# Performance work log

Measured on AMD Instinct MI355X. Metric: run time of the kernel, lower is better.

Reference implementation:

```python
import jax, jax.numpy as jnp
import numpy as np

EPS = 1e-6
BLK = 16  # NVFP4 block size (16 elements share one e4m3 scale)
# e2m1 representable magnitudes and rounding midpoints
GRID = jnp.array([0.0, 0.5, 1.0, 1.5, 2.0, 3.0, 4.0, 6.0], dtype=jnp.float32)
MID = jnp.array([0.25, 0.75, 1.25, 1.75, 2.5, 3.5, 5.0], dtype=jnp.float32)


def _e2m1(x):
    # round magnitude to nearest e2m1 grid point (saturate at 6.0)
    a = jnp.minimum(jnp.abs(x), 6.0)
    idx = jnp.searchsorted(MID, a, side='right')
    return jnp.sign(x) * jnp.take(GRID, idx)


def _fp4_quant_scaled(x, gscale):
    # vllm scaled_fp4_quant: per-16 block amax -> e4m3 block scale (scaled by
    # global scale), quantize to e2m1. Returns q * s8 (= dequant * gscale).
    m, n = x.shape
    xb = x.reshape(m, n // BLK, BLK)
    amax = jnp.max(jnp.abs(xb), axis=-1, keepdims=True)
    s8 = (amax * gscale / 6.0).astype(jnp.float8_e4m3fn).astype(jnp.float32)
    safe = jnp.where(s8 > 0, s8, 1.0)
    q = _e2m1(jnp.where(s8 > 0, xb * gscale / safe, 0.0))
    return (q * s8).reshape(m, n)


def _fp4_mm(y, w, ag, wg):
    # cutlass_scaled_fp4_mm with alpha = 1/(ag*wg): dequantized matmul y @ w.T
    alpha = 1.0 / (ag * wg)
    yq = _fp4_quant_scaled(y, ag)   # [m, h]
    wq = _fp4_quant_scaled(w, wg)   # [h, h]
    return (yq @ wq.T) * alpha


def _rmsnorm(x, w):
    v = jnp.mean(x * x, axis=-1, keepdims=True)
    return x * jax.lax.rsqrt(v + EPS) * w


def setup_inputs() -> dict:
    key = jax.random.key(0)
    k1, k2, k3, k4 = jax.random.split(key, 4)
    T, H = 8192, 4096
    hidden_states = jax.random.normal(k1, (T, H), dtype=jnp.float32)
    norm_w = jnp.ones((4, H), dtype=jnp.float32)          # RMSNorm weights (init ones)
    w = jax.random.uniform(k2, (3, H, H), dtype=jnp.float32)     # torch.rand
    agscale = jax.random.uniform(k3, (3,), dtype=jnp.float32, minval=0.25, maxval=1.0)
    wgscale = jax.random.uniform(k4, (3,), dtype=jnp.float32, minval=0.25, maxval=1.0)
    return {"hidden_states": hidden_states, "norm_w": norm_w, "w": w,
            "agscale": agscale, "wgscale": wgscale}


def reference(hidden_states, norm_w, w, agscale, wgscale):
    # tensor_model_parallel_all_reduce == identity on a single device
    x = jnp.maximum(hidden_states, 0.0)  # relu
    resid = x
    y = _rmsnorm(x, norm_w[0])
    for i in range(3):  # 3 structurally distinct layers (fixed small loop)
        z = _fp4_mm(y, w[i], agscale[i], wgscale[i])
        resid = z + resid                # fused add
        y = _rmsnorm(resid, norm_w[i + 1])
    return y
```

## Files before the change

kernel.cpp:

```cpp
#include <hip/hip_runtime.h>
#include <stdint.h>

#define HD 4096
#define TD 8192

typedef unsigned short u16;
typedef unsigned int u32;
typedef __bf16 bf16x8 __attribute__((ext_vector_type(8)));
typedef float f32x4 __attribute__((ext_vector_type(4)));

#define GL16(gp, lp) __builtin_amdgcn_global_load_lds( \
    (__attribute__((address_space(1))) void*)(void*)(uintptr_t)(gp), \
    (__attribute__((address_space(3))) void*)(lp), 16, 0, 0)


__device__ __forceinline__ float e4m3_rtne(float f) {
  if (f <= 0.0f) return 0.0f;
  unsigned u = __float_as_uint(f);
  int e = (int)((u >> 23) & 0xff) - 127;
  if (e < -6) e = -6;
  float C = __uint_as_float((unsigned)(e + 147) << 23);
  float r = (f + C) - C;
  return fminf(r, 448.0f);
}

__device__ __forceinline__ void quant_store16(const float v[16], float g, u16* dst) {
  float amax = 0.0f;
#pragma unroll
  for (int j = 0; j < 16; ++j) amax = fmaxf(amax, fabsf(v[j]));
  float s = e4m3_rtne(amax * g / 6.0f);
  u32 out[8];
  if (s > 0.0f) {
    const float m1 = 0.25f * s, m2 = 0.75f * s, m3 = 1.25f * s, m4 = 1.75f * s;
    const float m5 = 2.5f * s, m6 = 3.5f * s, m7 = 5.0f * s;
#pragma unroll
    for (int p = 0; p < 8; ++p) {
      u16 b[2];
#pragma unroll
      for (int h = 0; h < 2; ++h) {
        float t = v[2 * p + h] * g;
        float u = fabsf(t);
        float q = (u < m4) ? ((u < m2) ? ((u < m1) ? 0.0f : 0.5f)
                                       : ((u < m3) ? 1.0f : 1.5f))
                           : ((u < m6) ? ((u < m5) ? 2.0f : 3.0f)
                                       : ((u < m7) ? 4.0f : 6.0f));
        float val = copysignf(q * s, t);
        b[h] = (u16)(__float_as_uint(val) >> 16);
      }
      out[p] = (u32)b[0] | ((u32)b[1] << 16);
    }
  } else {
#pragma unroll
    for (int p = 0; p < 8; ++p) out[p] = 0u;
  }
  uint4* d4 = (uint4*)dst;
  d4[0] = make_uint4(out[0], out[1], out[2], out[3]);
  d4[1] = make_uint4(out[4], out[5], out[6], out[7]);
}

__device__ __forceinline__ float block_sum256(float v) {
#pragma unroll
  for (int off = 32; off > 0; off >>= 1) v += __shfl_down(v, off, 64);
  __shared__ float red[4];
  int tid = threadIdx.x;
  if ((tid & 63) == 0) red[tid >> 6] = v;
  __syncthreads();
  return (red[0] + red[1]) + (red[2] + red[3]);
}


__global__ __launch_bounds__(256) void k_relu_norm_quant(
    const float* __restrict__ hs, const float* __restrict__ nw,
    const float* __restrict__ agp, float* __restrict__ resid,
    u16* __restrict__ yq) {
  const int row = blockIdx.x, tid = threadIdx.x;
  const size_t base = (size_t)row * HD + tid * 16;
  float v[16];
#pragma unroll
  for (int j = 0; j < 4; ++j) ((float4*)v)[j] = ((const float4*)(hs + base))[j];
  float ss = 0.0f;
#pragma unroll
  for (int j = 0; j < 16; ++j) {
    v[j] = fmaxf(v[j], 0.0f);
    ss += v[j] * v[j];
  }
#pragma unroll
  for (int j = 0; j < 4; ++j) ((float4*)(resid + base))[j] = ((float4*)v)[j];
  float tot = block_sum256(ss);
  float rs = 1.0f / sqrtf(tot * (1.0f / HD) + 1e-6f);
  const float* nwp = nw + tid * 16;
  float y[16];
#pragma unroll
  for (int j = 0; j < 16; ++j) y[j] = v[j] * rs * nwp[j];
  quant_store16(y, agp[0], yq + base);
}

__global__ __launch_bounds__(256) void k_norm_quant(
    const float* __restrict__ resid, const float* __restrict__ nw,
    const float* __restrict__ agp, int li, u16* __restrict__ yq) {
  const int row = blockIdx.x, tid = threadIdx.x;
  const size_t base = (size_t)row * HD + tid * 16;
  float v[16];
#pragma unroll
  for (int j = 0; j < 4; ++j) ((float4*)v)[j] = ((const float4*)(resid + base))[j];
  float ss = 0.0f;
#pragma unroll
  for (int j = 0; j < 16; ++j) ss += v[j] * v[j];
  float tot = block_sum256(ss);
  float rs = 1.0f / sqrtf(tot * (1.0f / HD) + 1e-6f);
  const float* nwp = nw + (size_t)li * HD + tid * 16;
  float y[16];
#pragma unroll
  for (int j = 0; j < 16; ++j) y[j] = v[j] * rs * nwp[j];
  quant_store16(y, agp[li], yq + base);
}

__global__ __launch_bounds__(256) void k_final_norm(
    float* __restrict__ io, const float* __restrict__ nw) {
  const int row = blockIdx.x, tid = threadIdx.x;
  const size_t base = (size_t)row * HD + tid * 16;
  float v[16];
#pragma unroll
  for (int j = 0; j < 4; ++j) ((float4*)v)[j] = ((const float4*)(io + base))[j];
  float ss = 0.0f;
#pragma unroll
  for (int j = 0; j < 16; ++j) ss += v[j] * v[j];
  float tot = block_sum256(ss);
  float rs = 1.0f / sqrtf(tot * (1.0f / HD) + 1e-6f);
  const float* nwp = nw + (size_t)3 * HD + tid * 16;
#pragma unroll
  for (int j = 0; j < 16; ++j) v[j] = v[j] * rs * nwp[j];
#pragma unroll
  for (int j = 0; j < 4; ++j) ((float4*)(io + base))[j] = ((float4*)v)[j];
}

__global__ __launch_bounds__(256) void k_quant_w(
    const float* __restrict__ w, const float* __restrict__ wgp, int li,
    u16* __restrict__ wq) {
  const int row = blockIdx.x, tid = threadIdx.x;
  const size_t base = (size_t)li * HD * HD + (size_t)row * HD + tid * 16;
  float v[16];
#pragma unroll
  for (int j = 0; j < 4; ++j) ((float4*)v)[j] = ((const float4*)(w + base))[j];
  quant_store16(v, wgp[li], wq + (size_t)row * HD + tid * 16);
}


__global__ __launch_bounds__(256, 5) void k_gemm(
    const u16* __restrict__ A, const u16* __restrict__ B,
    float* __restrict__ resid, const float* __restrict__ agp,
    const float* __restrict__ wgp, int layer) {
  __shared__ __align__(16) u16 ldsA[128 * 32];
  __shared__ __align__(16) u16 ldsB[128 * 32];
  const int tid = threadIdx.x;
  const int wave = tid >> 6, lane = tid & 63;
  const int m0 = blockIdx.y * 128, n0 = blockIdx.x * 128;

  const int c0 = wave * 64 + lane;
  const int c1 = c0 + 256;
  const int rA0 = c0 >> 2, col0 = ((c0 & 3) ^ ((c0 >> 3) & 3)) * 8;
  const int rA1 = c1 >> 2, col1 = ((c1 & 3) ^ ((c1 >> 3) & 3)) * 8;

  const u16* gA0 = A + (size_t)(m0 + rA0) * HD + col0;
  const u16* gA1 = A + (size_t)(m0 + rA1) * HD + col1;
  const u16* gB0 = B + (size_t)(n0 + rA0) * HD + col0;
  const u16* gB1 = B + (size_t)(n0 + rA1) * HD + col1;
  u16* lA0 = ldsA + c0 * 8;
  u16* lA1 = ldsA + c1 * 8;
  u16* lB0 = ldsB + c0 * 8;
  u16* lB1 = ldsB + c1 * 8;

  const int wm = (wave >> 1) * 64, wn = (wave & 1) * 64;
  const int r = lane & 15, q = lane >> 4;
  const int sw = (q ^ ((r >> 1) & 3)) * 8;

  f32x4 acc[4][4];
#pragma unroll
  for (int i = 0; i < 4; ++i)
#pragma unroll
    for (int j = 0; j < 4; ++j) acc[i][j] = (f32x4){0.f, 0.f, 0.f, 0.f};

  for (int k0 = 0; k0 < HD; k0 += 32) {
    __syncthreads();
    GL16(gA0, lA0);
    GL16(gA1, lA1);
    GL16(gB0, lB0);
    GL16(gB1, lB1);
    gA0 += 32; gA1 += 32; gB0 += 32; gB1 += 32;
    __syncthreads();
    bf16x8 a[4], b[4];
#pragma unroll
    for (int i = 0; i < 4; ++i)
      a[i] = *(const bf16x8*)&ldsA[(wm + i * 16 + r) * 32 + sw];
#pragma unroll
    for (int j = 0; j < 4; ++j)
      b[j] = *(const bf16x8*)&ldsB[(wn + j * 16 + r) * 32 + sw];
#pragma unroll
    for (int i = 0; i < 4; ++i)
#pragma unroll
      for (int j = 0; j < 4; ++j)
        acc[i][j] = __builtin_amdgcn_mfma_f32_16x16x32_bf16(a[i], b[j], acc[i][j], 0, 0, 0);
  }

  const float alpha = 1.0f / (agp[layer] * wgp[layer]);
#pragma unroll
  for (int i = 0; i < 4; ++i) {
    const int gm0 = m0 + wm + i * 16 + q * 4;
#pragma unroll
    for (int j = 0; j < 4; ++j) {
      const int gn = n0 + wn + j * 16 + r;
#pragma unroll
      for (int t = 0; t < 4; ++t) {
        float* p = resid + (size_t)(gm0 + t) * HD + gn;
        *p = fmaf(acc[i][j][t], alpha, *p);
      }
    }
  }
}


extern "C" void kernel_launch(void* const* d_in, const int* in_sizes, int n_in,
                              void* d_out, int out_size, void* d_ws, size_t ws_size,
                              hipStream_t stream) {
  const float* hs = (const float*)d_in[0];
  const float* nw = (const float*)d_in[1];
  const float* w = (const float*)d_in[2];
  const float* ag = (const float*)d_in[3];
  const float* wg = (const float*)d_in[4];
  float* out = (float*)d_out;

  u16* wq = (u16*)d_ws;
  u16* yq = (u16*)d_ws + (size_t)HD * HD;

  k_relu_norm_quant<<<TD, 256, 0, stream>>>(hs, nw, ag, out, yq);
  for (int l = 0; l < 3; ++l) {
    k_quant_w<<<HD, 256, 0, stream>>>(w, wg, l, wq);
    k_gemm<<<dim3(HD / 128, TD / 128), 256, 0, stream>>>(yq, wq, out, ag, wg, l);
    if (l < 2) k_norm_quant<<<TD, 256, 0, stream>>>(out, nw, ag, l + 1, yq);
  }
  k_final_norm<<<TD, 256, 0, stream>>>(out, nw);
}
```

Measured before the change: 1.514 ms.

## Rewrite GEMM with 256x256 tiles, double-buffered LDS pipeline, and block swizzle

The bf16 MFMA GEMM moves from 128x128 tiles with K=32 steps and two full barriers per step to 256x256 tiles with 512 threads and K=64 half-tiles. Global-to-LDS loads are double-buffered and interleaved with MFMA phases using explicit waitcnt, barriers and setprio. Block IDs are remapped so neighbouring blocks reuse operands in L2. The aims are more data reuse per byte loaded, hiding load latency behind compute, and better cache locality. In exchange it uses 128KB of LDS and many registers, which limits occupancy, and the hand-written waitcnt and barrier schedule is fragile.

```diff
diff --git a/kernel.cpp b/kernel.cpp
--- a/kernel.cpp
+++ b/kernel.cpp
@@ -146,73 +146,143 @@
 }
 
 
-__global__ __launch_bounds__(256, 5) void k_gemm(
+#define BARF() do { asm volatile("" ::: "memory"); \
+    __builtin_amdgcn_s_barrier(); \
+    asm volatile("" ::: "memory"); } while (0)
+#define WLG() asm volatile("s_waitcnt lgkmcnt(0)" ::: "memory")
+#define WVM6() asm volatile("s_waitcnt vmcnt(6)" ::: "memory")
+
+__global__ __launch_bounds__(512, 2) void k_gemm(
     const u16* __restrict__ A, const u16* __restrict__ B,
     float* __restrict__ resid, const float* __restrict__ agp,
     const float* __restrict__ wgp, int layer) {
-  __shared__ __align__(16) u16 ldsA[128 * 32];
-  __shared__ __align__(16) u16 ldsB[128 * 32];
+  __shared__ __align__(16) u16 ldsA[2 * 256 * 64];
+  __shared__ __align__(16) u16 ldsB[2 * 256 * 64];
   const int tid = threadIdx.x;
-  const int wave = tid >> 6, lane = tid & 63;
-  const int m0 = blockIdx.y * 128, n0 = blockIdx.x * 128;
-
-  const int c0 = wave * 64 + lane;
-  const int c1 = c0 + 256;
-  const int rA0 = c0 >> 2, col0 = ((c0 & 3) ^ ((c0 >> 3) & 3)) * 8;
-  const int rA1 = c1 >> 2, col1 = ((c1 & 3) ^ ((c1 >> 3) & 3)) * 8;
-
-  const u16* gA0 = A + (size_t)(m0 + rA0) * HD + col0;
-  const u16* gA1 = A + (size_t)(m0 + rA1) * HD + col1;
-  const u16* gB0 = B + (size_t)(n0 + rA0) * HD + col0;
-  const u16* gB1 = B + (size_t)(n0 + rA1) * HD + col1;
-  u16* lA0 = ldsA + c0 * 8;
-  u16* lA1 = ldsA + c1 * 8;
-  u16* lB0 = ldsB + c0 * 8;
-  u16* lB1 = ldsB + c1 * 8;
-
-  const int wm = (wave >> 1) * 64, wn = (wave & 1) * 64;
+  const int lane = tid & 63, wave = tid >> 6;
+  const int wr = wave >> 2, wc = wave & 3;
   const int r = lane & 15, q = lane >> 4;
-  const int sw = (q ^ ((r >> 1) & 3)) * 8;
-
-  f32x4 acc[4][4];
-#pragma unroll
-  for (int i = 0; i < 4; ++i)
+
+  int bid = blockIdx.x;
+  bid = (bid & 7) * 64 + (bid >> 3);
+  const int m0 = (bid >> 4) * 256;
+  const int n0 = (bid & 15) * 256;
+
+  const int rs = tid >> 3;
+  const int cs = ((tid & 7) ^ (rs & 7)) * 8;
+  const u16* gA = A + (size_t)(m0 + rs) * HD + cs;
+  const u16* gB = B + (size_t)(n0 + rs) * HD + cs;
+  u16* lA = ldsA + tid * 8;
+  u16* lB = ldsB + tid * 8;
+
+#define STG_A(bb, h, koff) do { \
+    GL16(gA + (size_t)(h) * (128 * HD) + (koff), lA + (bb) + (h) * 8192); \
+    GL16(gA + (size_t)(h) * (128 * HD) + 64 * HD + (koff), lA + (bb) + (h) * 8192 + 4096); \
+  } while (0)
+#define STG_B(bb, h, koff) do { \
+    GL16(gB + (size_t)(h) * (128 * HD) + (koff), lB + (bb) + (h) * 8192); \
+    GL16(gB + (size_t)(h) * (128 * HD) + 64 * HD + (koff), lB + (bb) + (h) * 8192 + 4096); \
+  } while (0)
+
+  const int sa = (q ^ (r & 7)) * 8;
+  const int sb = ((q + 4) ^ (r & 7)) * 8;
+  const int arow = (wr * 128 + r) * 64;
+  const int brow = (wc * 64 + r) * 64;
+
+  f32x4 acc[8][4];
+#pragma unroll
+  for (int i = 0; i < 8; ++i)
 #pragma unroll
     for (int j = 0; j < 4; ++j) acc[i][j] = (f32x4){0.f, 0.f, 0.f, 0.f};
 
-  for (int k0 = 0; k0 < HD; k0 += 32) {
-    __syncthreads();
-    GL16(gA0, lA0);
-    GL16(gA1, lA1);
-    GL16(gB0, lB0);
-    GL16(gB1, lB1);
-    gA0 += 32; gA1 += 32; gB0 += 32; gB1 += 32;
-    __syncthreads();
-    bf16x8 a[4], b[4];
-#pragma unroll
-    for (int i = 0; i < 4; ++i)
-      a[i] = *(const bf16x8*)&ldsA[(wm + i * 16 + r) * 32 + sw];
-#pragma unroll
-    for (int j = 0; j < 4; ++j)
-      b[j] = *(const bf16x8*)&ldsB[(wn + j * 16 + r) * 32 + sw];
-#pragma unroll
-    for (int i = 0; i < 4; ++i)
-#pragma unroll
-      for (int j = 0; j < 4; ++j)
-        acc[i][j] = __builtin_amdgcn_mfma_f32_16x16x32_bf16(a[i], b[j], acc[i][j], 0, 0, 0);
+  bf16x8 a[4][2], b[4][2];
+
+#define LD_A(base) do { \
+    _Pragma("unroll") \
+    for (int mi = 0; mi < 4; ++mi) { \
+      a[mi][0] = *(const bf16x8*)((base) + arow + mi * 1024 + sa); \
+      a[mi][1] = *(const bf16x8*)((base) + arow + mi * 1024 + sb); \
+    } } while (0)
+#define LD_B(base) do { \
+    _Pragma("unroll") \
+    for (int nj = 0; nj < 4; ++nj) { \
+      b[nj][0] = *(const bf16x8*)((base) + brow + nj * 1024 + sa); \
+      b[nj][1] = *(const bf16x8*)((base) + brow + nj * 1024 + sb); \
+    } } while (0)
+#define MMQ(mh, nh) do { \
+    _Pragma("unroll") \
+    for (int mi = 0; mi < 4; ++mi) \
+    _Pragma("unroll") \
+    for (int nj = 0; nj < 2; ++nj) { \
+      acc[(mh) * 4 + mi][(nh) * 2 + nj] = __builtin_amdgcn_mfma_f32_16x16x32_bf16( \
+          a[mi][0], b[(nh) * 2 + nj][0], acc[(mh) * 4 + mi][(nh) * 2 + nj], 0, 0, 0); \
+      acc[(mh) * 4 + mi][(nh) * 2 + nj] = __builtin_amdgcn_mfma_f32_16x16x32_bf16( \
+          a[mi][1], b[(nh) * 2 + nj][1], acc[(mh) * 4 + mi][(nh) * 2 + nj], 0, 0, 0); \
+    } } while (0)
+
+  STG_B(0, 0, 0); STG_B(0, 1, 0);
+  STG_A(0, 0, 0); STG_A(0, 1, 0);
+  STG_B(16384, 0, 64); STG_B(16384, 1, 64);
+  STG_A(16384, 0, 64);
+  WVM6();
+  BARF();
+
+  for (int i = 0; i < 32; ++i) {
+    const int kb = i * 128;
+    const int k1 = kb + 64;
+    int k2 = kb + 128; if (k2 >= HD) k2 -= HD;
+    int k3 = kb + 192; if (k3 >= HD) k3 -= HD;
+    LD_A(ldsA); LD_B(ldsB);
+    STG_A(16384, 1, k1);
+    BARF(); WLG();
+    __builtin_amdgcn_s_setprio(1); MMQ(0, 0); __builtin_amdgcn_s_setprio(0);
+    BARF();
+    STG_B(0, 0, k2);
+    BARF();
+    __builtin_amdgcn_s_setprio(1); MMQ(0, 1); __builtin_amdgcn_s_setprio(0);
+    BARF();
+    LD_A(ldsA + 4096);
+    STG_B(0, 1, k2);
+    BARF(); WLG();
+    __builtin_amdgcn_s_setprio(1); MMQ(1, 0); __builtin_amdgcn_s_setprio(0);
+    BARF();
+    STG_A(0, 0, k2);
+    WVM6();
+    BARF();
+    __builtin_amdgcn_s_setprio(1); MMQ(1, 1); __builtin_amdgcn_s_setprio(0);
+    BARF();
+    LD_A(ldsA + 16384); LD_B(ldsB + 16384);
+    STG_A(0, 1, k2);
+    BARF(); WLG();
+    __builtin_amdgcn_s_setprio(1); MMQ(0, 0); __builtin_amdgcn_s_setprio(0);
+    BARF();
+    STG_B(16384, 0, k3);
+    BARF();
+    __builtin_amdgcn_s_setprio(1); MMQ(0, 1); __builtin_amdgcn_s_setprio(0);
+    BARF();
+    LD_A(ldsA + 16384 + 4096);
+    STG_B(16384, 1, k3);
+    BARF(); WLG();
+    __builtin_amdgcn_s_setprio(1); MMQ(1, 0); __builtin_amdgcn_s_setprio(0);
+    BARF();
+    STG_A(16384, 0, k3);
+    WVM6();
+    BARF();
+    __builtin_amdgcn_s_setprio(1); MMQ(1, 1); __builtin_amdgcn_s_setprio(0);
+    BARF();
   }
 
   const float alpha = 1.0f / (agp[layer] * wgp[layer]);
 #pragma unroll
-  for (int i = 0; i < 4; ++i) {
-    const int gm0 = m0 + wm + i * 16 + q * 4;
-#pragma unroll
-    for (int j = 0; j < 4; ++j) {
-      const int gn = n0 + wn + j * 16 + r;
+  for (int mi = 0; mi < 8; ++mi) {
+    const int gm0 = m0 + wr * 128 + mi * 16 + q * 4;
+#pragma unroll
+    for (int nj = 0; nj < 4; ++nj) {
+      const int gn = n0 + wc * 64 + nj * 16 + r;
 #pragma unroll
       for (int t = 0; t < 4; ++t) {
         float* p = resid + (size_t)(gm0 + t) * HD + gn;
-        *p = fmaf(acc[i][j][t], alpha, *p);
+        *p = fmaf(acc[mi][nj][t], alpha, *p);
       }
     }
   }
@@ -235,7 +305,7 @@
   k_relu_norm_quant<<<TD, 256, 0, stream>>>(hs, nw, ag, out, yq);
   for (int l = 0; l < 3; ++l) {
     k_quant_w<<<HD, 256, 0, stream>>>(w, wg, l, wq);
-    k_gemm<<<dim3(HD / 128, TD / 128), 256, 0, stream>>>(yq, wq, out, ag, wg, l);
+    k_gemm<<<dim3((TD / 256) * (HD / 256)), 512, 0, stream>>>(yq, wq, out, ag, wg, l);
     if (l < 2) k_norm_quant<<<TD, 256, 0, stream>>>(out, nw, ag, l + 1, yq);
   }
   k_final_norm<<<TD, 256, 0, stream>>>(out, nw);
```

After: 1.325 ms. -12.5%, faster.
